# Kernel tuning notes

Measured on AMD Instinct MI355X. Metric: run time of the kernel, lower is better.

The kernel has to match this reference:

```python
import jax, jax.numpy as jnp
import numpy as np

B, N, NFG, NFR = 512, 64, 1024, 256
OH, OW = 87, 157
POS_THRESHOLD = 0.2


def setup_inputs() -> dict:
    key = jax.random.key(0)
    ks = jax.random.split(key, 7)
    feats = jax.random.normal(ks[0], (B, N, NFG), dtype=jnp.float32)
    # boxes (x1,y1,x2,y2) in image coordinates
    boxes = jax.random.uniform(ks[1], (B, N, 4), dtype=jnp.float32)
    scale = jnp.array([OW, OH, OW, OH], dtype=jnp.float32)
    boxes = boxes * scale
    s_in = 1.0 / np.sqrt(NFG)
    W_theta = jax.random.normal(ks[2], (NFG, NFR), dtype=jnp.float32) * s_in
    b_theta = jnp.zeros((NFR,), dtype=jnp.float32)
    W_phi = jax.random.normal(ks[3], (NFG, NFR), dtype=jnp.float32) * s_in
    b_phi = jnp.zeros((NFR,), dtype=jnp.float32)
    W_gcn = jax.random.normal(ks[4], (NFG, NFG), dtype=jnp.float32) * s_in
    return {
        "graph_boxes_features": feats,
        "boxes_in_flat": boxes,
        "W_theta": W_theta,
        "b_theta": b_theta,
        "W_phi": W_phi,
        "b_phi": b_phi,
        "W_gcn": W_gcn,
    }


def reference(graph_boxes_features, boxes_in_flat, W_theta, b_theta, W_phi, b_phi, W_gcn):
    nfr = W_theta.shape[-1]
    # box centers [B,N,2]
    cx = (boxes_in_flat[..., 0] + boxes_in_flat[..., 2]) * 0.5
    cy = (boxes_in_flat[..., 1] + boxes_in_flat[..., 3]) * 0.5
    pos = jnp.stack([cx, cy], axis=-1)  # [B,N,2]
    # pairwise euclidean distances [B,N,N]
    diff = pos[:, :, None, :] - pos[:, None, :, :]
    dist = jnp.sqrt(jnp.sum(diff * diff, axis=-1))
    position_mask = dist > (POS_THRESHOLD * OW)

    theta = jnp.einsum('bnf,fr->bnr', graph_boxes_features, W_theta) + b_theta
    phi = jnp.einsum('bnf,fr->bnr', graph_boxes_features, W_phi) + b_phi
    sim = jnp.einsum('bnr,bmr->bnm', theta, phi) / jnp.sqrt(jnp.asarray(nfr, theta.dtype))
    logits = jnp.where(position_mask, -jnp.inf, sim)
    relation_graph = jax.nn.softmax(logits, axis=2)  # [B,N,N]

    agg = jnp.einsum('bnm,bmf->bnf', relation_graph, graph_boxes_features)
    out = jax.nn.relu(jnp.einsum('bnf,fg->bng', agg, W_gcn))
    return out, relation_graph
```

## Files before the change

### kernel.cpp

```cpp
#include <hip/hip_runtime.h>
#include <hip/hip_bf16.h>
#include <math.h>

#define BB   512
#define NN   64
#define NFG  1024
#define NFR  256
#define MM   (BB * NN)
#define RG_OFF 33554432L

typedef __attribute__((ext_vector_type(8))) short bf16x8;
typedef __attribute__((ext_vector_type(4))) float f32x4;
typedef __attribute__((ext_vector_type(8))) unsigned short u16x8;
typedef __attribute__((ext_vector_type(4))) unsigned short u16x4;

__device__ inline unsigned short f2bf(float f) {
    union { float f; unsigned u; } v; v.f = f;
    unsigned u = v.u;
    return (unsigned short)((u + 0x7FFFu + ((u >> 16) & 1u)) >> 16);
}

__device__ inline void gld_lds16(const unsigned short* g, unsigned short* l) {
    __builtin_amdgcn_global_load_lds((const __attribute__((address_space(1))) void*)g,
                                     (__attribute__((address_space(3))) void*)l, 16, 0, 0);
}


__global__ __launch_bounds__(256) void cast_f32_bf16(const float* __restrict__ in,
                                                     unsigned short* __restrict__ out, long n) {
    long i = ((long)blockIdx.x * 256 + threadIdx.x) * 8;
    if (i + 8 <= n) {
        f32x4 a = *(const f32x4*)(in + i);
        f32x4 b = *(const f32x4*)(in + i + 4);
        u16x8 o;
#pragma unroll
        for (int c = 0; c < 4; ++c) { o[c] = f2bf(a[c]); o[4 + c] = f2bf(b[c]); }
        *(u16x8*)(out + i) = o;
    }
}

__global__ void transpose_cast(const float* __restrict__ in, unsigned short* __restrict__ out,
                               int K, int N) {
    __shared__ float tile[32][33];
    int tx = threadIdx.x, ty = threadIdx.y;
    int k0 = blockIdx.y * 32, n0 = blockIdx.x * 32;
#pragma unroll
    for (int r = 0; r < 4; ++r)
        tile[ty + r * 8][tx] = in[(long)(k0 + ty + r * 8) * N + n0 + tx];
    __syncthreads();
#pragma unroll
    for (int r = 0; r < 4; ++r)
        out[(long)(n0 + ty + r * 8) * K + k0 + tx] = f2bf(tile[tx][ty + r * 8]);
}

__global__ void concat_bias(const float* __restrict__ bt, const float* __restrict__ bp,
                            float* __restrict__ out) {
    int i = threadIdx.x;
    out[i] = (i < 256) ? bt[i] : bp[i - 256];
}


template<int RELU, int OUT_MODE>
__global__ __launch_bounds__(256)
void gemm_bt(const unsigned short* __restrict__ A, const unsigned short* __restrict__ Bt,
             const float* __restrict__ bias, void* __restrict__ Cout,
             int M, int N, int K) {
    __shared__ __align__(16) unsigned short As[128 * 32];
    __shared__ __align__(16) unsigned short Bs[128 * 32];
    const int t    = threadIdx.x;
    const int lane = t & 63;
    const int w    = t >> 6;
    const int l15  = lane & 15;
    const int q    = lane >> 4;
    const long tileM = (long)blockIdx.x * 128;
    const long tileN = (long)blockIdx.y * 128;
    const int wm = (w & 1) * 64;
    const int wn = (w >> 1) * 64;

    f32x4 acc[4][4] = {};

    const int rS = t >> 2;
    const int cS = t & 3;
    const unsigned short* gA0 = A  + (tileM + rS) * (long)K + cS * 8;
    const unsigned short* gA1 = gA0 + 64L * K;
    const unsigned short* gB0 = Bt + (tileN + rS) * (long)K + cS * 8;
    const unsigned short* gB1 = gB0 + 64L * K;
    unsigned short* lA0 = As + (0 * 256 + w * 64) * 8;
    unsigned short* lA1 = As + (1 * 256 + w * 64) * 8;
    unsigned short* lB0 = Bs + (0 * 256 + w * 64) * 8;
    unsigned short* lB1 = Bs + (1 * 256 + w * 64) * 8;

    for (int kt = 0; kt < K; kt += 32) {
        __syncthreads();
        gld_lds16(gA0 + kt, lA0);
        gld_lds16(gA1 + kt, lA1);
        gld_lds16(gB0 + kt, lB0);
        gld_lds16(gB1 + kt, lB1);
        __syncthreads();
        bf16x8 af[4], bf[4];
#pragma unroll
        for (int mi = 0; mi < 4; ++mi)
            af[mi] = *(const bf16x8*)(As + (wm + mi * 16 + l15) * 32 + q * 8);
#pragma unroll
        for (int ni = 0; ni < 4; ++ni)
            bf[ni] = *(const bf16x8*)(Bs + (wn + ni * 16 + l15) * 32 + q * 8);
#pragma unroll
        for (int mi = 0; mi < 4; ++mi)
#pragma unroll
            for (int ni = 0; ni < 4; ++ni)
                acc[mi][ni] = __builtin_amdgcn_mfma_f32_16x16x32_bf16(af[mi], bf[ni],
                                                                      acc[mi][ni], 0, 0, 0);
    }

#pragma unroll
    for (int mi = 0; mi < 4; ++mi) {
#pragma unroll
        for (int ni = 0; ni < 4; ++ni) {
            long row0 = tileM + wm + mi * 16 + q * 4;
            long col  = tileN + wn + ni * 16 + l15;
            float bv = bias ? bias[col] : 0.f;
            if (OUT_MODE == 2) {
                u16x4 o;
#pragma unroll
                for (int r = 0; r < 4; ++r) {
                    float v = acc[mi][ni][r] + bv;
                    if (RELU) v = fmaxf(v, 0.f);
                    o[r] = f2bf(v);
                }
                long base = (row0 >> 6) * ((long)N * 64) + col * 64 + (row0 & 63);
                *(u16x4*)((unsigned short*)Cout + base) = o;
            } else {
#pragma unroll
                for (int r = 0; r < 4; ++r) {
                    float v = acc[mi][ni][r] + bv;
                    if (RELU) v = fmaxf(v, 0.f);
                    long idx = (row0 + r) * N + col;
                    if (OUT_MODE == 1) ((unsigned short*)Cout)[idx] = f2bf(v);
                    else               ((float*)Cout)[idx] = v;
                }
            }
        }
    }
}


__global__ __launch_bounds__(256)
void fused_softmax_out(const unsigned short* __restrict__ thetaphi,
                       const float* __restrict__ boxes,
                       const unsigned short* __restrict__ Ht,
                       float* __restrict__ rg_out,
                       float* __restrict__ out) {
    __shared__ __align__(16) float sim_s[64][68];
    __shared__ __align__(16) unsigned short Pb[64][72];
    __shared__ float cxs[64], cys[64];
    const int t    = threadIdx.x;
    const int b    = blockIdx.x;
    const int lane = t & 63;
    const int w    = t >> 6;
    const int l15  = lane & 15;
    const int q    = lane >> 4;

    if (t < 64) {
        float4 bx = *(const float4*)(boxes + ((long)b * 64 + t) * 4);
        cxs[t] = (bx.x + bx.z) * 0.5f;
        cys[t] = (bx.y + bx.w) * 0.5f;
    }

    {
        f32x4 acc[4] = {};
        const unsigned short* thA = thetaphi + ((long)b * 64 + w * 16 + l15) * 512 + q * 8;
        const unsigned short* thB = thetaphi + ((long)b * 64 + l15) * 512 + 256 + q * 8;
#pragma unroll
        for (int kt = 0; kt < 256; kt += 32) {
            bf16x8 a = *(const bf16x8*)(thA + kt);
#pragma unroll
            for (int ni = 0; ni < 4; ++ni) {
                bf16x8 bb = *(const bf16x8*)(thB + (long)ni * 16 * 512 + kt);
                acc[ni] = __builtin_amdgcn_mfma_f32_16x16x32_bf16(a, bb, acc[ni], 0, 0, 0);
            }
        }
#pragma unroll
        for (int ni = 0; ni < 4; ++ni)
#pragma unroll
            for (int r = 0; r < 4; ++r)
                sim_s[w * 16 + q * 4 + r][ni * 16 + l15] = acc[ni][r] * 0.0625f;
    }
    __syncthreads();

    {
        const int i  = t >> 2;
        const int j0 = (t & 3) * 16;
        const float cxi = cxs[i], cyi = cys[i];
        const float thr = (float)(0.2 * 157.0);
        float vals[16];
        float mx = -__builtin_inff();
#pragma unroll
        for (int jj = 0; jj < 16; ++jj) {
            int j = j0 + jj;
            float dx = cxi - cxs[j];
            float dy = cyi - cys[j];
            bool msk = sqrtf(dx * dx + dy * dy) > thr;
            float s = msk ? -__builtin_inff() : sim_s[i][j];
            vals[jj] = s;
            mx = fmaxf(mx, s);
        }
        mx = fmaxf(mx, __shfl_xor(mx, 1, 64));
        mx = fmaxf(mx, __shfl_xor(mx, 2, 64));
        float sum = 0.f;
#pragma unroll
        for (int jj = 0; jj < 16; ++jj) {
            float e = (vals[jj] == -__builtin_inff()) ? 0.f : __expf(vals[jj] - mx);
            vals[jj] = e;
            sum += e;
        }
        sum += __shfl_xor(sum, 1, 64);
        sum += __shfl_xor(sum, 2, 64);
        float inv = 1.f / sum;
#pragma unroll
        for (int jj = 0; jj < 16; ++jj) {
            int j = j0 + jj;
            float p = vals[jj] * inv;
            rg_out[((long)b * 64 + i) * 64 + j] = p;
            Pb[i][j] = f2bf(p);
        }
    }
    __syncthreads();

    {
        const unsigned short* HtB = Ht + (long)b * 65536;
        float* outB = out + (long)b * 65536;
        bf16x8 af[4][2];
#pragma unroll
        for (int mi = 0; mi < 4; ++mi)
#pragma unroll
            for (int kk = 0; kk < 2; ++kk)
                af[mi][kk] = *(const bf16x8*)(&Pb[mi * 16 + l15][kk * 32 + q * 8]);
#pragma unroll 2
        for (int nt = 0; nt < 16; ++nt) {
            const int g0 = w * 256 + nt * 16;
            const unsigned short* hp = HtB + (long)(g0 + l15) * 64 + q * 8;
            bf16x8 b0 = *(const bf16x8*)(hp);
            bf16x8 b1 = *(const bf16x8*)(hp + 32);
#pragma unroll
            for (int mi = 0; mi < 4; ++mi) {
                f32x4 acc = {};
                acc = __builtin_amdgcn_mfma_f32_16x16x32_bf16(af[mi][0], b0, acc, 0, 0, 0);
                acc = __builtin_amdgcn_mfma_f32_16x16x32_bf16(af[mi][1], b1, acc, 0, 0, 0);
#pragma unroll
                for (int r = 0; r < 4; ++r)
                    outB[(long)(mi * 16 + q * 4 + r) * 1024 + g0 + l15] = fmaxf(acc[r], 0.f);
            }
        }
    }
}


extern "C" void kernel_launch(void* const* d_in, const int* in_sizes, int n_in,
                              void* d_out, int out_size, void* d_ws, size_t ws_size,
                              hipStream_t stream) {
    const float* feats   = (const float*)d_in[0];
    const float* boxes   = (const float*)d_in[1];
    const float* W_theta = (const float*)d_in[2];
    const float* b_theta = (const float*)d_in[3];
    const float* W_phi   = (const float*)d_in[4];
    const float* b_phi   = (const float*)d_in[5];
    const float* W_gcn   = (const float*)d_in[6];
    float* out = (float*)d_out;

    char* ws = (char*)d_ws;
    unsigned short* featsb   = (unsigned short*)(ws);
    unsigned short* thetaphi = (unsigned short*)(ws + 67108864);
    unsigned short* Ht       = (unsigned short*)(ws + 100663296);
    unsigned short* Wtp      = (unsigned short*)(ws + 167772160);
    unsigned short* Wgt      = (unsigned short*)(ws + 168820736);
    float*          bias512  = (float*)(ws + 170917888);

    cast_f32_bf16<<<16384, 256, 0, stream>>>(feats, featsb, 33554432L);
    transpose_cast<<<dim3(8, 32),  dim3(32, 8), 0, stream>>>(W_theta, Wtp,              1024, 256);
    transpose_cast<<<dim3(8, 32),  dim3(32, 8), 0, stream>>>(W_phi,   Wtp + 256 * 1024, 1024, 256);
    transpose_cast<<<dim3(32, 32), dim3(32, 8), 0, stream>>>(W_gcn,   Wgt,              1024, 1024);
    concat_bias<<<1, 512, 0, stream>>>(b_theta, b_phi, bias512);

    gemm_bt<0, 1><<<dim3(256, 4), 256, 0, stream>>>(featsb, Wtp, bias512, thetaphi,
                                                    MM, 512, 1024);
    gemm_bt<0, 2><<<dim3(256, 8), 256, 0, stream>>>(featsb, Wgt, nullptr, Ht,
                                                    MM, 1024, 1024);
    fused_softmax_out<<<BB, 256, 0, stream>>>(thetaphi, boxes, Ht, out + RG_OFF, out);
}
```

Measured before the change: 498.0 us.

## Deepen GEMM k-tile to 64 with XOR-swizzled LDS and swap H GEMM operands

The GEMM now stages 64-wide k slices per iteration, halving the number of barrier pairs. It applies an XOR swizzle to the LDS column slots to avoid bank conflicts on the fragment reads. The H = feats·W_gcn GEMM is computed transposed (W_gcn as the A operand), so it writes H^T in plain row-major bf16 and the special blocked output mode is removed. The softmax kernel reads H^T with a 32768-element stride per feature row, which gives strided global reads in exchange for contiguous GEMM stores and larger LDS use.

```diff
diff --git a/kernel.cpp b/kernel.cpp
--- a/kernel.cpp
+++ b/kernel.cpp
@@ -12,7 +12,6 @@
 typedef __attribute__((ext_vector_type(8))) short bf16x8;
 typedef __attribute__((ext_vector_type(4))) float f32x4;
 typedef __attribute__((ext_vector_type(8))) unsigned short u16x8;
-typedef __attribute__((ext_vector_type(4))) unsigned short u16x4;
 
 __device__ inline unsigned short f2bf(float f) {
     union { float f; unsigned u; } v; v.f = f;
@@ -60,13 +59,13 @@
 }
 
 
-template<int RELU, int OUT_MODE>
+template<int RELU, int STORE_BF16>
 __global__ __launch_bounds__(256)
 void gemm_bt(const unsigned short* __restrict__ A, const unsigned short* __restrict__ Bt,
              const float* __restrict__ bias, void* __restrict__ Cout,
              int M, int N, int K) {
-    __shared__ __align__(16) unsigned short As[128 * 32];
-    __shared__ __align__(16) unsigned short Bs[128 * 32];
+    __shared__ __align__(16) unsigned short As[128 * 64];
+    __shared__ __align__(16) unsigned short Bs[128 * 64];
     const int t    = threadIdx.x;
     const int lane = t & 63;
     const int w    = t >> 6;
@@ -79,37 +78,36 @@
 
     f32x4 acc[4][4] = {};
 
-    const int rS = t >> 2;
-    const int cS = t & 3;
-    const unsigned short* gA0 = A  + (tileM + rS) * (long)K + cS * 8;
-    const unsigned short* gA1 = gA0 + 64L * K;
-    const unsigned short* gB0 = Bt + (tileN + rS) * (long)K + cS * 8;
-    const unsigned short* gB1 = gB0 + 64L * K;
-    unsigned short* lA0 = As + (0 * 256 + w * 64) * 8;
-    unsigned short* lA1 = As + (1 * 256 + w * 64) * 8;
-    unsigned short* lB0 = Bs + (0 * 256 + w * 64) * 8;
-    unsigned short* lB1 = Bs + (1 * 256 + w * 64) * 8;
-
-    for (int kt = 0; kt < K; kt += 32) {
+    const int rS = t >> 3;
+    const int cS = (t & 7) ^ (rS & 7);
+    const unsigned short* gA = A  + (tileM + rS) * (long)K + cS * 8;
+    const unsigned short* gB = Bt + (tileN + rS) * (long)K + cS * 8;
+
+    for (int kt = 0; kt < K; kt += 64) {
         __syncthreads();
-        gld_lds16(gA0 + kt, lA0);
-        gld_lds16(gA1 + kt, lA1);
-        gld_lds16(gB0 + kt, lB0);
-        gld_lds16(gB1 + kt, lB1);
+#pragma unroll
+        for (int i = 0; i < 4; ++i) {
+            gld_lds16(gA + (long)i * 32 * K + kt, As + (i * 256 + w * 64) * 8);
+            gld_lds16(gB + (long)i * 32 * K + kt, Bs + (i * 256 + w * 64) * 8);
+        }
         __syncthreads();
-        bf16x8 af[4], bf[4];
-#pragma unroll
-        for (int mi = 0; mi < 4; ++mi)
-            af[mi] = *(const bf16x8*)(As + (wm + mi * 16 + l15) * 32 + q * 8);
-#pragma unroll
-        for (int ni = 0; ni < 4; ++ni)
-            bf[ni] = *(const bf16x8*)(Bs + (wn + ni * 16 + l15) * 32 + q * 8);
-#pragma unroll
-        for (int mi = 0; mi < 4; ++mi)
+#pragma unroll
+        for (int ks = 0; ks < 2; ++ks) {
+            const int slot = (ks * 4 + q) ^ (l15 & 7);
+            bf16x8 af[4], bf[4];
+#pragma unroll
+            for (int mi = 0; mi < 4; ++mi)
+                af[mi] = *(const bf16x8*)(As + (wm + mi * 16 + l15) * 64 + slot * 8);
 #pragma unroll
             for (int ni = 0; ni < 4; ++ni)
-                acc[mi][ni] = __builtin_amdgcn_mfma_f32_16x16x32_bf16(af[mi], bf[ni],
-                                                                      acc[mi][ni], 0, 0, 0);
+                bf[ni] = *(const bf16x8*)(Bs + (wn + ni * 16 + l15) * 64 + slot * 8);
+#pragma unroll
+            for (int mi = 0; mi < 4; ++mi)
+#pragma unroll
+                for (int ni = 0; ni < 4; ++ni)
+                    acc[mi][ni] = __builtin_amdgcn_mfma_f32_16x16x32_bf16(af[mi], bf[ni],
+                                                                          acc[mi][ni], 0, 0, 0);
+        }
     }
 
 #pragma unroll
@@ -119,25 +117,13 @@
             long row0 = tileM + wm + mi * 16 + q * 4;
             long col  = tileN + wn + ni * 16 + l15;
             float bv = bias ? bias[col] : 0.f;
-            if (OUT_MODE == 2) {
-                u16x4 o;
-#pragma unroll
-                for (int r = 0; r < 4; ++r) {
-                    float v = acc[mi][ni][r] + bv;
-                    if (RELU) v = fmaxf(v, 0.f);
-                    o[r] = f2bf(v);
-                }
-                long base = (row0 >> 6) * ((long)N * 64) + col * 64 + (row0 & 63);
-                *(u16x4*)((unsigned short*)Cout + base) = o;
-            } else {
-#pragma unroll
-                for (int r = 0; r < 4; ++r) {
-                    float v = acc[mi][ni][r] + bv;
-                    if (RELU) v = fmaxf(v, 0.f);
-                    long idx = (row0 + r) * N + col;
-                    if (OUT_MODE == 1) ((unsigned short*)Cout)[idx] = f2bf(v);
-                    else               ((float*)Cout)[idx] = v;
-                }
+#pragma unroll
+            for (int r = 0; r < 4; ++r) {
+                float v = acc[mi][ni][r] + bv;
+                if (RELU) v = fmaxf(v, 0.f);
+                long idx = (row0 + r) * N + col;
+                if (STORE_BF16) ((unsigned short*)Cout)[idx] = f2bf(v);
+                else            ((float*)Cout)[idx] = v;
             }
         }
     }
@@ -147,7 +133,7 @@
 __global__ __launch_bounds__(256)
 void fused_softmax_out(const unsigned short* __restrict__ thetaphi,
                        const float* __restrict__ boxes,
-                       const unsigned short* __restrict__ Ht,
+                       const unsigned short* __restrict__ HtT,
                        float* __restrict__ rg_out,
                        float* __restrict__ out) {
     __shared__ __align__(16) float sim_s[64][68];
@@ -227,7 +213,7 @@
     __syncthreads();
 
     {
-        const unsigned short* HtB = Ht + (long)b * 65536;
+        const unsigned short* HtB = HtT + (long)b * 64;
         float* outB = out + (long)b * 65536;
         bf16x8 af[4][2];
 #pragma unroll
@@ -238,7 +224,7 @@
 #pragma unroll 2
         for (int nt = 0; nt < 16; ++nt) {
             const int g0 = w * 256 + nt * 16;
-            const unsigned short* hp = HtB + (long)(g0 + l15) * 64 + q * 8;
+            const unsigned short* hp = HtB + (long)(g0 + l15) * 32768 + q * 8;
             bf16x8 b0 = *(const bf16x8*)(hp);
             bf16x8 b1 = *(const bf16x8*)(hp + 32);
 #pragma unroll
@@ -270,7 +256,7 @@
     char* ws = (char*)d_ws;
     unsigned short* featsb   = (unsigned short*)(ws);
     unsigned short* thetaphi = (unsigned short*)(ws + 67108864);
-    unsigned short* Ht       = (unsigned short*)(ws + 100663296);
+    unsigned short* HtT      = (unsigned short*)(ws + 100663296);
     unsigned short* Wtp      = (unsigned short*)(ws + 167772160);
     unsigned short* Wgt      = (unsigned short*)(ws + 168820736);
     float*          bias512  = (float*)(ws + 170917888);
@@ -283,7 +269,7 @@
 
     gemm_bt<0, 1><<<dim3(256, 4), 256, 0, stream>>>(featsb, Wtp, bias512, thetaphi,
                                                     MM, 512, 1024);
-    gemm_bt<0, 2><<<dim3(256, 8), 256, 0, stream>>>(featsb, Wgt, nullptr, Ht,
-                                                    MM, 1024, 1024);
-    fused_softmax_out<<<BB, 256, 0, stream>>>(thetaphi, boxes, Ht, out + RG_OFF, out);
-}
+    gemm_bt<0, 1><<<dim3(8, 256), 256, 0, stream>>>(Wgt, featsb, nullptr, HtT,
+                                                    1024, MM, 1024);
+    fused_softmax_out<<<BB, 256, 0, stream>>>(thetaphi, boxes, HtT, out + RG_OFF, out);
+}
```

Result: faster. 473.8 us (-4.9%).
